# Kernel optimization log

Measured on AMD Instinct MI355X. Metric: run time of the kernel, lower is better.

Reference implementation:

```python
import jax, jax.numpy as jnp
import numpy as np

HIDDEN = 800
BETA = 0.95
SLOPE = 25.0

@jax.custom_vjp
def surrogate_spike(mem, thr):
    # hard threshold forward, sigmoid-derivative surrogate backward
    return (mem > thr).astype(mem.dtype)

def _spk_fwd(mem, thr):
    return surrogate_spike(mem, thr), (mem, thr)

def _spk_bwd(res, g):
    mem, thr = res
    s = jax.nn.sigmoid(SLOPE * (mem - thr))
    return (g * SLOPE * s * (1.0 - s), jnp.zeros_like(thr))

surrogate_spike.defvjp(_spk_fwd, _spk_bwd)


def setup_inputs() -> dict:
    key = jax.random.key(0)
    ks = jax.random.split(key, 6)
    T, B = 50, 512
    x = jax.random.normal(ks[0], (T, B, 784), dtype=jnp.float32)
    # Kaiming-ish init scaled by 1/sqrt(fan_in)
    W1 = jax.random.normal(ks[1], (HIDDEN, 784), dtype=jnp.float32) / np.sqrt(784.0)
    W2 = jax.random.normal(ks[2], (HIDDEN, HIDDEN), dtype=jnp.float32) / np.sqrt(float(HIDDEN))
    W3 = jax.random.normal(ks[3], (10, HIDDEN), dtype=jnp.float32) / np.sqrt(float(HIDDEN))
    b1 = jnp.zeros((HIDDEN,), jnp.float32)
    b2 = jnp.zeros((HIDDEN,), jnp.float32)
    b3 = jnp.zeros((10,), jnp.float32)
    budget1 = jax.random.uniform(ks[4], (HIDDEN,), dtype=jnp.float32)
    budget2 = jax.random.uniform(ks[5], (HIDDEN,), dtype=jnp.float32)
    return {"x": x, "W1": W1, "b1": b1, "W2": W2, "b2": b2,
            "W3": W3, "b3": b3, "budget1": budget1, "budget2": budget2}


def reference(x, W1, b1, W2, b2, W3, b3, budget1, budget2):
    # thresholds: 1 / clamp(budget / max_budget, 0.01, 1.0); max_budget = 1.0 here
    thr1 = 1.0 / jnp.clip(budget1, 0.01, 1.0)
    thr2 = 1.0 / jnp.clip(budget2, 0.01, 1.0)
    thr3 = jnp.asarray(1.0, x.dtype)
    B = x.shape[1]

    def step(carry, xt):
        m1, m2, m3 = carry
        m1 = BETA * m1 + xt @ W1.T + b1            # [B, HIDDEN]
        s1 = surrogate_spike(m1, thr1)
        m1 = m1 * (1.0 - s1)                        # multiplicative reset
        m2 = BETA * m2 + s1 @ W2.T + b2
        s2 = surrogate_spike(m2, thr2)
        m2 = m2 * (1.0 - s2)
        m3 = BETA * m3 + s2 @ W3.T + b3            # [B, 10]
        s3 = surrogate_spike(m3, thr3)
        m3 = m3 * (1.0 - s3)
        return (m1, m2, m3), (s1, s2, s3)

    init = (jnp.zeros((B, HIDDEN), x.dtype),
            jnp.zeros((B, HIDDEN), x.dtype),
            jnp.zeros((B, 10), x.dtype))
    _, (s1r, s2r, s3r) = jax.lax.scan(step, init, x)
    return (s3r.sum(0), s1r, s2r, s3r)
```

## Files before the change

kernel.cpp:

```cpp
#include <hip/hip_runtime.h>

#define BATCH   512
#define TSTEPS  50
#define NIN     784
#define NHID    800
#define NOUT    10
#define KC      384

typedef float v4f __attribute__((ext_vector_type(4)));

__global__ __launch_bounds__(256, 2)
void gemm_panel_f32(const float* __restrict__ A, const float* __restrict__ B,
                    float* __restrict__ Cp, int M, int N, int K,
                    int ks, int ke)
{
    __shared__ float As[8][132];
    __shared__ float Bs[8][188];

    const int tid = threadIdx.x;
    const int tx = tid & 15;
    const int ty = tid >> 4;
    const int m0 = blockIdx.x * 128;
    const int n0 = blockIdx.y * 128;

    const int srow = tid >> 1;
    const int skq  = (tid & 1) * 4;
    const int bphys = 12 * (srow >> 3) + (srow & 7);

    const float* Aptr = A + (size_t)(m0 + srow) * K + skq;
    const float* Bptr = B + (size_t)(n0 + srow) * K + skq;
    const bool bval = (n0 + srow) < N;

    float part[8][8];
    #pragma unroll
    for (int i = 0; i < 8; ++i)
        #pragma unroll
        for (int j = 0; j < 8; ++j) part[i][j] = 0.0f;

    float4 av = *(const float4*)(Aptr + ks);
    float4 bv = bval ? *(const float4*)(Bptr + ks) : make_float4(0.f,0.f,0.f,0.f);

    for (int k0 = ks; k0 < ke; k0 += 8) {
        __syncthreads();
        As[skq+0][srow] = av.x; As[skq+1][srow] = av.y;
        As[skq+2][srow] = av.z; As[skq+3][srow] = av.w;
        Bs[skq+0][bphys] = bv.x; Bs[skq+1][bphys] = bv.y;
        Bs[skq+2][bphys] = bv.z; Bs[skq+3][bphys] = bv.w;
        __syncthreads();

        if (k0 + 8 < ke) {
            av = *(const float4*)(Aptr + k0 + 8);
            bv = bval ? *(const float4*)(Bptr + k0 + 8)
                      : make_float4(0.f,0.f,0.f,0.f);
        }

        #pragma unroll
        for (int kk = 0; kk < 8; ++kk) {
            float a[8], b[8];
            *(float4*)&a[0] = *(const float4*)&As[kk][8*ty];
            *(float4*)&a[4] = *(const float4*)&As[kk][8*ty + 4];
            *(float4*)&b[0] = *(const float4*)&Bs[kk][12*tx];
            *(float4*)&b[4] = *(const float4*)&Bs[kk][12*tx + 4];
            #pragma unroll
            for (int i = 0; i < 8; ++i)
                #pragma unroll
                for (int j = 0; j < 8; ++j)
                    part[i][j] = __fmaf_rn(a[i], b[j], part[i][j]);
        }
    }

    const int cb = n0 + 8 * tx;
    #pragma unroll
    for (int i = 0; i < 8; ++i) {
        float* crow = Cp + (size_t)(m0 + 8*ty + i) * N + cb;
        if (cb + 4 <= N) {
            v4f o = { part[i][0], part[i][1], part[i][2], part[i][3] };
            __builtin_nontemporal_store(o, (v4f*)crow);
        }
        if (cb + 8 <= N) {
            v4f o = { part[i][4], part[i][5], part[i][6], part[i][7] };
            __builtin_nontemporal_store(o, (v4f*)(crow + 4));
        }
    }
}

__global__ __launch_bounds__(256)
void transpose800(const float* __restrict__ W2, float* __restrict__ W2T)
{
    __shared__ float t[32][33];
    const int tx  = threadIdx.x & 31;
    const int ty8 = threadIdx.x >> 5;
    const int bx = blockIdx.x * 32, by = blockIdx.y * 32;

    #pragma unroll
    for (int r = 0; r < 4; ++r) {
        int a = ty8 + r * 8;
        t[a][tx] = W2[(size_t)(by + a) * 800 + bx + tx];
    }
    __syncthreads();
    #pragma unroll
    for (int r = 0; r < 4; ++r) {
        int a = ty8 + r * 8;
        W2T[(size_t)(bx + a) * 800 + by + tx] = t[tx][a];
    }
}

__global__ __launch_bounds__(256)
void lif_scan_hid(const float* __restrict__ Z0,
                  const float* __restrict__ Z1,
                  const float* __restrict__ Z2,
                  int np,
                  const float* __restrict__ bias,
                  const float* __restrict__ budget,
                  float* __restrict__ mcarry,
                  float* __restrict__ Sout,
                  unsigned long long* __restrict__ bm,
                  int CT, int t0)
{
    const int b = blockIdx.x;
    const int tid = threadIdx.x;
    const int lane = tid & 63;
    const int wave = tid >> 6;

    float m[4], thr[4], bj[4];
    bool val[4];
    #pragma unroll
    for (int c = 0; c < 4; ++c) {
        const int j = c * 256 + tid;
        val[c] = (j < NHID);
        const int jj = val[c] ? j : 0;
        float bu = budget[jj];
        bu = fminf(fmaxf(bu, 0.01f), 1.0f);
        thr[c] = __fdiv_rn(1.0f, bu);
        bj[c]  = bias[jj];
        m[c]   = mcarry[b * NHID + jj];
    }

    for (int ct = 0; ct < CT; ++ct) {
        const size_t zbase = (size_t)ct * (BATCH * NHID) + (size_t)b * NHID;
        const size_t sbase = (size_t)(t0 + ct) * (BATCH * NHID) + (size_t)b * NHID;
        #pragma unroll
        for (int c = 0; c < 4; ++c) {
            const int j = c * 256 + tid;
            bool sp = false;
            if (val[c]) {
                float z = __builtin_nontemporal_load(Z0 + zbase + j);
                if (np >= 2)
                    z = __fadd_rn(z, __builtin_nontemporal_load(Z1 + zbase + j));
                if (np >= 3)
                    z = __fadd_rn(z, __builtin_nontemporal_load(Z2 + zbase + j));
                float mm = __fadd_rn(__fadd_rn(__fmul_rn(0.95f, m[c]), z), bj[c]);
                sp = (mm > thr[c]);
                m[c] = sp ? 0.0f : mm;
                __builtin_nontemporal_store(sp ? 1.0f : 0.0f, Sout + sbase + j);
            }
            unsigned long long bits = __ballot(sp);
            if (bm && lane == 0) {
                const int W = c * 4 + wave;
                if (W < 13)
                    bm[((size_t)ct * BATCH + b) * 13 + W] = bits;
            }
        }
    }
    #pragma unroll
    for (int c = 0; c < 4; ++c)
        if (val[c]) mcarry[b * NHID + c * 256 + tid] = m[c];
}

__global__ __launch_bounds__(256)
void spmm_spikes(const unsigned long long* __restrict__ bm,
                 const float* __restrict__ W2T,
                 float* __restrict__ Z,
                 int rows)
{
    __shared__ unsigned long long wbuf[13];
    __shared__ unsigned short list[NHID];
    __shared__ int offs[14];

    const int tid = threadIdx.x;
    const int lane = tid & 63;
    const int wave = tid >> 6;
    const int row = blockIdx.x;

    if (tid < 13) wbuf[tid] = bm[(size_t)row * 13 + tid];
    __syncthreads();
    if (tid == 0) {
        int o = 0;
        for (int w = 0; w < 13; ++w) { offs[w] = o; o += __popcll(wbuf[w]); }
        offs[13] = o;
    }
    __syncthreads();
    for (int W = wave; W < 13; W += 4) {
        const unsigned long long bits = wbuf[W];
        const int pre = __popcll(bits & ((1ull << lane) - 1ull));
        if ((bits >> lane) & 1ull)
            list[offs[W] + pre] = (unsigned short)(W * 64 + lane);
    }
    __syncthreads();
    const int nnz = offs[13];

    if (tid < 200) {
        const int n = 4 * tid;
        float p0 = 0.f, p1 = 0.f, p2 = 0.f, p3 = 0.f;
        float a0 = 0.f, a1 = 0.f, a2 = 0.f, a3 = 0.f;
        int p = 0, nextb = KC;
        for (int i = 0; i < nnz; ++i) {
            const int k = list[i];
            while (k >= nextb) {
                if (p == 0) { a0 = p0; a1 = p1; a2 = p2; a3 = p3; }
                else {
                    a0 = __fadd_rn(a0, p0); a1 = __fadd_rn(a1, p1);
                    a2 = __fadd_rn(a2, p2); a3 = __fadd_rn(a3, p3);
                }
                p0 = p1 = p2 = p3 = 0.f; ++p;
                nextb = (nextb == KC) ? 2 * KC : 100000;
            }
            const float4 w = *(const float4*)(W2T + (size_t)k * NHID + n);
            p0 = __fadd_rn(p0, w.x); p1 = __fadd_rn(p1, w.y);
            p2 = __fadd_rn(p2, w.z); p3 = __fadd_rn(p3, w.w);
        }
        while (p < 3) {
            if (p == 0) { a0 = p0; a1 = p1; a2 = p2; a3 = p3; }
            else {
                a0 = __fadd_rn(a0, p0); a1 = __fadd_rn(a1, p1);
                a2 = __fadd_rn(a2, p2); a3 = __fadd_rn(a3, p3);
            }
            p0 = p1 = p2 = p3 = 0.f; ++p;
        }
        *(float4*)(Z + (size_t)row * NHID + n) = make_float4(a0, a1, a2, a3);
    }
}

__global__ __launch_bounds__(256)
void gemm3_f32(const float* __restrict__ S2, const float* __restrict__ W3,
               float* __restrict__ Z3, int rows)
{
    int gid = blockIdx.x * 256 + threadIdx.x;
    if (gid >= rows * NOUT) return;
    const int m = gid / NOUT;
    const int nn = gid % NOUT;
    const float* a = S2 + (size_t)m * NHID;
    const float* wr = W3 + (size_t)nn * NHID;

    float part = 0.0f, acc = 0.0f;
    int p = 0;
    for (int i = 0; i < NHID / 4; ++i) {
        if (i == 96 || i == 192) {
            acc = (p == 0) ? part : __fadd_rn(acc, part);
            part = 0.0f; ++p;
        }
        const v4f a4 = __builtin_nontemporal_load((const v4f*)(a + 4 * i));
        const float4 w4 = *(const float4*)(wr + 4 * i);
        part = __fmaf_rn(a4.x, w4.x, part);
        part = __fmaf_rn(a4.y, w4.y, part);
        part = __fmaf_rn(a4.z, w4.z, part);
        part = __fmaf_rn(a4.w, w4.w, part);
    }
    acc = (p == 0) ? part : __fadd_rn(acc, part);
    Z3[gid] = acc;
}

__global__ __launch_bounds__(256)
void lif_scan_small(const float* __restrict__ Z, const float* __restrict__ bias,
                    float* __restrict__ mcarry, float* __restrict__ Sout,
                    int CT, int t0)
{
    const int idx = blockIdx.x * blockDim.x + threadIdx.x;
    const int total = BATCH * NOUT;
    if (idx >= total) return;
    const int j = idx % NOUT;
    const float thr = 1.0f;
    const float bj = bias[j];

    float m = mcarry[idx];
    for (int ct = 0; ct < CT; ++ct) {
        float z = Z[(size_t)ct * total + idx];
        m = __fadd_rn(__fadd_rn(__fmul_rn(0.95f, m), z), bj);
        float s;
        if (m > thr) { s = 1.0f; m = 0.0f; }
        else         { s = 0.0f; }
        Sout[(size_t)(t0 + ct) * total + idx] = s;
    }
    mcarry[idx] = m;
}

__global__ __launch_bounds__(256)
void sum_t(const float* __restrict__ S3, float* __restrict__ out0)
{
    const int idx = blockIdx.x * blockDim.x + threadIdx.x;
    if (idx >= BATCH * NOUT) return;
    float s = 0.0f;
    for (int t = 0; t < TSTEPS; ++t)
        s += S3[(size_t)t * BATCH * NOUT + idx];
    out0[idx] = s;
}

extern "C" void kernel_launch(void* const* d_in, const int* in_sizes, int n_in,
                              void* d_out, int out_size, void* d_ws, size_t ws_size,
                              hipStream_t stream)
{
    const float* x       = (const float*)d_in[0];
    const float* W1      = (const float*)d_in[1];
    const float* b1      = (const float*)d_in[2];
    const float* W2      = (const float*)d_in[3];
    const float* b2      = (const float*)d_in[4];
    const float* W3      = (const float*)d_in[5];
    const float* b3      = (const float*)d_in[6];
    const float* budget1 = (const float*)d_in[7];
    const float* budget2 = (const float*)d_in[8];

    float* out  = (float*)d_out;
    float* out0 = out;
    float* out1 = out0 + BATCH * NOUT;
    float* out2 = out1 + (size_t)TSTEPS * BATCH * NHID;
    float* out3 = out2 + (size_t)TSTEPS * BATCH * NHID;

    const size_t nBH = (size_t)BATCH * NHID;
    const size_t nBO = (size_t)BATCH * NOUT;
    float* m1c = (float*)d_ws;
    float* m2c = m1c + nBH;
    float* m3c = m2c + nBH;
    float* w2t = m3c + nBO;
    unsigned long long* bmask = (unsigned long long*)(w2t + (size_t)NHID * NHID);
    float* Z = (float*)(bmask + (size_t)TSTEPS * BATCH * 13);

    const size_t fixedF = 2 * nBH + nBO + (size_t)NHID * NHID
                        + (size_t)TSTEPS * BATCH * 13 * 2;
    size_t availF = (ws_size / 4 > fixedF) ? (ws_size / 4 - fixedF) : 0;
    const size_t perT = (size_t)BATCH * (3 * NHID + NOUT);
    int CT = (int)(availF / perT);
    if (CT > TSTEPS) CT = TSTEPS;
    if (CT < 1) CT = 1;

    hipMemsetAsync(d_ws, 0, (2 * nBH + nBO) * sizeof(float), stream);

    {
        dim3 tg(25, 25);
        transpose800<<<tg, 256, 0, stream>>>(W2, w2t);
    }

    for (int t0 = 0; t0 < TSTEPS; t0 += CT) {
        int ct = TSTEPS - t0 < CT ? TSTEPS - t0 : CT;
        int Mrows = ct * BATCH;
        const size_t pstride = (size_t)ct * BATCH * NHID;
        float* Zp0 = Z;
        float* Zp1 = Z + pstride;
        float* Zp2 = Z + 2 * pstride;
        float* Z3  = Z + 3 * pstride;

        {
            dim3 grid(Mrows / 128, (NHID + 127) / 128);
            const float* xc = x + (size_t)t0 * BATCH * NIN;
            gemm_panel_f32<<<grid, 256, 0, stream>>>(xc, W1, Zp0, Mrows, NHID, NIN, 0,   384);
            gemm_panel_f32<<<grid, 256, 0, stream>>>(xc, W1, Zp1, Mrows, NHID, NIN, 384, 768);
            gemm_panel_f32<<<grid, 256, 0, stream>>>(xc, W1, Zp2, Mrows, NHID, NIN, 768, 784);
        }
        lif_scan_hid<<<BATCH, 256, 0, stream>>>(
            Zp0, Zp1, Zp2, 3, b1, budget1, m1c, out1, bmask, ct, t0);

        spmm_spikes<<<Mrows, 256, 0, stream>>>(bmask, w2t, Zp0, Mrows);
        lif_scan_hid<<<BATCH, 256, 0, stream>>>(
            Zp0, nullptr, nullptr, 1, b2, budget2, m2c, out2, nullptr, ct, t0);

        gemm3_f32<<<(Mrows * NOUT + 255) / 256, 256, 0, stream>>>(
            out2 + (size_t)t0 * BATCH * NHID, W3, Z3, Mrows);
        lif_scan_small<<<(BATCH * NOUT + 255) / 256, 256, 0, stream>>>(
            Z3, b3, m3c, out3, ct, t0);
    }

    sum_t<<<(BATCH * NOUT + 255) / 256, 256, 0, stream>>>(out3, out0);
}
```

Baseline: 1.006 ms.

## Fuse W1 K-tail into layer-1 scan and drop third partial panel

The 16-column tail of the x·W1ᵀ GEMM (k 768–784) is no longer run as a separate gemm_panel launch writing a full [T·B,800] partial buffer. Instead lif_scan_hid1 stages that W1 slice in shared memory and computes the 16-term dot product inline before the membrane update. This removes one launch plus a full-size write and read of partial sums, and frees workspace so CT can grow. Separately, the GEMM accumulators are rewritten as float4 pairs and the output stores become regular instead of nontemporal. The scan now does extra FMAs and shared loads per element and uses about 54KB of LDS per block, which may limit occupancy.

```diff
diff --git a/kernel.cpp b/kernel.cpp
--- a/kernel.cpp
+++ b/kernel.cpp
@@ -9,6 +9,21 @@
 
 typedef float v4f __attribute__((ext_vector_type(4)));
 
+#define ROW_FMA(pl, ph, as)                       \
+    pl.x = __fmaf_rn(as, blo.x, pl.x);            \
+    pl.y = __fmaf_rn(as, blo.y, pl.y);            \
+    pl.z = __fmaf_rn(as, blo.z, pl.z);            \
+    pl.w = __fmaf_rn(as, blo.w, pl.w);            \
+    ph.x = __fmaf_rn(as, bhi.x, ph.x);            \
+    ph.y = __fmaf_rn(as, bhi.y, ph.y);            \
+    ph.z = __fmaf_rn(as, bhi.z, ph.z);            \
+    ph.w = __fmaf_rn(as, bhi.w, ph.w);
+
+#define STORE_ROW(i, pl, ph)                                        \
+    {   float* crow = Cp + (size_t)(m0 + 8*ty + (i)) * N + cb;      \
+        if (cb + 4 <= N) *(float4*)crow = pl;                       \
+        if (cb + 8 <= N) *(float4*)(crow + 4) = ph; }
+
 __global__ __launch_bounds__(256, 2)
 void gemm_panel_f32(const float* __restrict__ A, const float* __restrict__ B,
                     float* __restrict__ Cp, int M, int N, int K,
@@ -31,11 +46,10 @@
     const float* Bptr = B + (size_t)(n0 + srow) * K + skq;
     const bool bval = (n0 + srow) < N;
 
-    float part[8][8];
-    #pragma unroll
-    for (int i = 0; i < 8; ++i)
-        #pragma unroll
-        for (int j = 0; j < 8; ++j) part[i][j] = 0.0f;
+    float4 p0l = {0,0,0,0}, p0h = {0,0,0,0}, p1l = {0,0,0,0}, p1h = {0,0,0,0};
+    float4 p2l = {0,0,0,0}, p2h = {0,0,0,0}, p3l = {0,0,0,0}, p3h = {0,0,0,0};
+    float4 p4l = {0,0,0,0}, p4h = {0,0,0,0}, p5l = {0,0,0,0}, p5h = {0,0,0,0};
+    float4 p6l = {0,0,0,0}, p6h = {0,0,0,0}, p7l = {0,0,0,0}, p7h = {0,0,0,0};
 
     float4 av = *(const float4*)(Aptr + ks);
     float4 bv = bval ? *(const float4*)(Bptr + ks) : make_float4(0.f,0.f,0.f,0.f);
@@ -56,32 +70,30 @@
 
         #pragma unroll
         for (int kk = 0; kk < 8; ++kk) {
-            float a[8], b[8];
-            *(float4*)&a[0] = *(const float4*)&As[kk][8*ty];
-            *(float4*)&a[4] = *(const float4*)&As[kk][8*ty + 4];
-            *(float4*)&b[0] = *(const float4*)&Bs[kk][12*tx];
-            *(float4*)&b[4] = *(const float4*)&Bs[kk][12*tx + 4];
-            #pragma unroll
-            for (int i = 0; i < 8; ++i)
-                #pragma unroll
-                for (int j = 0; j < 8; ++j)
-                    part[i][j] = __fmaf_rn(a[i], b[j], part[i][j]);
+            const float4 alo = *(const float4*)&As[kk][8*ty];
+            const float4 ahi = *(const float4*)&As[kk][8*ty + 4];
+            const float4 blo = *(const float4*)&Bs[kk][12*tx];
+            const float4 bhi = *(const float4*)&Bs[kk][12*tx + 4];
+            ROW_FMA(p0l, p0h, alo.x)
+            ROW_FMA(p1l, p1h, alo.y)
+            ROW_FMA(p2l, p2h, alo.z)
+            ROW_FMA(p3l, p3h, alo.w)
+            ROW_FMA(p4l, p4h, ahi.x)
+            ROW_FMA(p5l, p5h, ahi.y)
+            ROW_FMA(p6l, p6h, ahi.z)
+            ROW_FMA(p7l, p7h, ahi.w)
         }
     }
 
     const int cb = n0 + 8 * tx;
-    #pragma unroll
-    for (int i = 0; i < 8; ++i) {
-        float* crow = Cp + (size_t)(m0 + 8*ty + i) * N + cb;
-        if (cb + 4 <= N) {
-            v4f o = { part[i][0], part[i][1], part[i][2], part[i][3] };
-            __builtin_nontemporal_store(o, (v4f*)crow);
-        }
-        if (cb + 8 <= N) {
-            v4f o = { part[i][4], part[i][5], part[i][6], part[i][7] };
-            __builtin_nontemporal_store(o, (v4f*)(crow + 4));
-        }
-    }
+    STORE_ROW(0, p0l, p0h)
+    STORE_ROW(1, p1l, p1h)
+    STORE_ROW(2, p2l, p2h)
+    STORE_ROW(3, p3l, p3h)
+    STORE_ROW(4, p4l, p4h)
+    STORE_ROW(5, p5l, p5h)
+    STORE_ROW(6, p6l, p6h)
+    STORE_ROW(7, p7l, p7h)
 }
 
 __global__ __launch_bounds__(256)
@@ -106,21 +118,108 @@
 }
 
 __global__ __launch_bounds__(256)
-void lif_scan_hid(const float* __restrict__ Z0,
-                  const float* __restrict__ Z1,
-                  const float* __restrict__ Z2,
-                  int np,
-                  const float* __restrict__ bias,
-                  const float* __restrict__ budget,
-                  float* __restrict__ mcarry,
-                  float* __restrict__ Sout,
-                  unsigned long long* __restrict__ bm,
-                  int CT, int t0)
-{
+void lif_scan_hid1(const float* __restrict__ Z0,
+                   const float* __restrict__ Z1,
+                   const float* __restrict__ xc,
+                   const float* __restrict__ W1,
+                   const float* __restrict__ bias,
+                   const float* __restrict__ budget,
+                   float* __restrict__ mcarry,
+                   float* __restrict__ Sout,
+                   unsigned long long* __restrict__ bm,
+                   int CT, int t0)
+{
+    __shared__ float W1s[NHID][17];
+
     const int b = blockIdx.x;
     const int tid = threadIdx.x;
     const int lane = tid & 63;
     const int wave = tid >> 6;
+
+    for (int q = tid; q < NHID * 16; q += 256)
+        W1s[q >> 4][q & 15] = W1[(size_t)(q >> 4) * NIN + 768 + (q & 15)];
+    __syncthreads();
+
+    float m[4], thr[4], bj[4];
+    bool val[4];
+    int jjv[4];
+    #pragma unroll
+    for (int c = 0; c < 4; ++c) {
+        const int j = c * 256 + tid;
+        val[c] = (j < NHID);
+        const int jj = val[c] ? j : 0;
+        jjv[c] = jj;
+        float bu = budget[jj];
+        bu = fminf(fmaxf(bu, 0.01f), 1.0f);
+        thr[c] = __fdiv_rn(1.0f, bu);
+        bj[c]  = bias[jj];
+        m[c]   = mcarry[b * NHID + jj];
+    }
+
+    for (int ct = 0; ct < CT; ++ct) {
+        const size_t zbase = (size_t)ct * (BATCH * NHID) + (size_t)b * NHID;
+        const size_t sbase = (size_t)(t0 + ct) * (BATCH * NHID) + (size_t)b * NHID;
+        const float* xr = xc + ((size_t)ct * BATCH + b) * NIN + 768;
+        const float4 x0 = *(const float4*)(xr);
+        const float4 x1 = *(const float4*)(xr + 4);
+        const float4 x2 = *(const float4*)(xr + 8);
+        const float4 x3 = *(const float4*)(xr + 12);
+
+        #pragma unroll
+        for (int c = 0; c < 4; ++c) {
+            const int j = c * 256 + tid;
+            bool sp = false;
+            if (val[c]) {
+                const int jj = jjv[c];
+                float z = __fadd_rn(__builtin_nontemporal_load(Z0 + zbase + j),
+                                    __builtin_nontemporal_load(Z1 + zbase + j));
+                float p3 = 0.0f;
+                p3 = __fmaf_rn(x0.x, W1s[jj][0],  p3);
+                p3 = __fmaf_rn(x0.y, W1s[jj][1],  p3);
+                p3 = __fmaf_rn(x0.z, W1s[jj][2],  p3);
+                p3 = __fmaf_rn(x0.w, W1s[jj][3],  p3);
+                p3 = __fmaf_rn(x1.x, W1s[jj][4],  p3);
+                p3 = __fmaf_rn(x1.y, W1s[jj][5],  p3);
+                p3 = __fmaf_rn(x1.z, W1s[jj][6],  p3);
+                p3 = __fmaf_rn(x1.w, W1s[jj][7],  p3);
+                p3 = __fmaf_rn(x2.x, W1s[jj][8],  p3);
+                p3 = __fmaf_rn(x2.y, W1s[jj][9],  p3);
+                p3 = __fmaf_rn(x2.z, W1s[jj][10], p3);
+                p3 = __fmaf_rn(x2.w, W1s[jj][11], p3);
+                p3 = __fmaf_rn(x3.x, W1s[jj][12], p3);
+                p3 = __fmaf_rn(x3.y, W1s[jj][13], p3);
+                p3 = __fmaf_rn(x3.z, W1s[jj][14], p3);
+                p3 = __fmaf_rn(x3.w, W1s[jj][15], p3);
+                z = __fadd_rn(z, p3);
+
+                float mm = __fadd_rn(__fadd_rn(__fmul_rn(0.95f, m[c]), z), bj[c]);
+                sp = (mm > thr[c]);
+                m[c] = sp ? 0.0f : mm;
+                __builtin_nontemporal_store(sp ? 1.0f : 0.0f, Sout + sbase + j);
+            }
+            unsigned long long bits = __ballot(sp);
+            if (lane == 0) {
+                const int W = c * 4 + wave;
+                if (W < 13)
+                    bm[((size_t)ct * BATCH + b) * 13 + W] = bits;
+            }
+        }
+    }
+    #pragma unroll
+    for (int c = 0; c < 4; ++c)
+        if (val[c]) mcarry[b * NHID + c * 256 + tid] = m[c];
+}
+
+__global__ __launch_bounds__(256)
+void lif_scan_hid2(const float* __restrict__ Z0,
+                   const float* __restrict__ bias,
+                   const float* __restrict__ budget,
+                   float* __restrict__ mcarry,
+                   float* __restrict__ Sout,
+                   int CT, int t0)
+{
+    const int b = blockIdx.x;
+    const int tid = threadIdx.x;
 
     float m[4], thr[4], bj[4];
     bool val[4];
@@ -142,23 +241,12 @@
         #pragma unroll
         for (int c = 0; c < 4; ++c) {
             const int j = c * 256 + tid;
-            bool sp = false;
             if (val[c]) {
                 float z = __builtin_nontemporal_load(Z0 + zbase + j);
-                if (np >= 2)
-                    z = __fadd_rn(z, __builtin_nontemporal_load(Z1 + zbase + j));
-                if (np >= 3)
-                    z = __fadd_rn(z, __builtin_nontemporal_load(Z2 + zbase + j));
                 float mm = __fadd_rn(__fadd_rn(__fmul_rn(0.95f, m[c]), z), bj[c]);
-                sp = (mm > thr[c]);
+                bool sp = (mm > thr[c]);
                 m[c] = sp ? 0.0f : mm;
                 __builtin_nontemporal_store(sp ? 1.0f : 0.0f, Sout + sbase + j);
-            }
-            unsigned long long bits = __ballot(sp);
-            if (bm && lane == 0) {
-                const int W = c * 4 + wave;
-                if (W < 13)
-                    bm[((size_t)ct * BATCH + b) * 13 + W] = bits;
             }
         }
     }
@@ -327,7 +415,7 @@
     const size_t fixedF = 2 * nBH + nBO + (size_t)NHID * NHID
                         + (size_t)TSTEPS * BATCH * 13 * 2;
     size_t availF = (ws_size / 4 > fixedF) ? (ws_size / 4 - fixedF) : 0;
-    const size_t perT = (size_t)BATCH * (3 * NHID + NOUT);
+    const size_t perT = (size_t)BATCH * (2 * NHID + NOUT);
     int CT = (int)(availF / perT);
     if (CT > TSTEPS) CT = TSTEPS;
     if (CT < 1) CT = 1;
@@ -345,22 +433,20 @@
         const size_t pstride = (size_t)ct * BATCH * NHID;
         float* Zp0 = Z;
         float* Zp1 = Z + pstride;
-        float* Zp2 = Z + 2 * pstride;
-        float* Z3  = Z + 3 * pstride;
+        float* Z3  = Z + 2 * pstride;
+        const float* xc = x + (size_t)t0 * BATCH * NIN;
 
         {
             dim3 grid(Mrows / 128, (NHID + 127) / 128);
-            const float* xc = x + (size_t)t0 * BATCH * NIN;
             gemm_panel_f32<<<grid, 256, 0, stream>>>(xc, W1, Zp0, Mrows, NHID, NIN, 0,   384);
             gemm_panel_f32<<<grid, 256, 0, stream>>>(xc, W1, Zp1, Mrows, NHID, NIN, 384, 768);
-            gemm_panel_f32<<<grid, 256, 0, stream>>>(xc, W1, Zp2, Mrows, NHID, NIN, 768, 784);
-        }
-        lif_scan_hid<<<BATCH, 256, 0, stream>>>(
-            Zp0, Zp1, Zp2, 3, b1, budget1, m1c, out1, bmask, ct, t0);
+        }
+        lif_scan_hid1<<<BATCH, 256, 0, stream>>>(
+            Zp0, Zp1, xc, W1, b1, budget1, m1c, out1, bmask, ct, t0);
 
         spmm_spikes<<<Mrows, 256, 0, stream>>>(bmask, w2t, Zp0, Mrows);
-        lif_scan_hid<<<BATCH, 256, 0, stream>>>(
-            Zp0, nullptr, nullptr, 1, b2, budget2, m2c, out2, nullptr, ct, t0);
+        lif_scan_hid2<<<BATCH, 256, 0, stream>>>(
+            Zp0, b2, budget2, m2c, out2, ct, t0);
 
         gemm3_f32<<<(Mrows * NOUT + 255) / 256, 256, 0, stream>>>(
             out2 + (size_t)t0 * BATCH * NHID, W3, Z3, Mrows);
```

New measurement: 840.4 us. -16.5%, faster.
